# Performance work log

Hardware: AMD Instinct MI355X
Metric: run time of the kernel (lower is better)

The kernel has to match this reference:

```python
import jax, jax.numpy as jnp
import numpy as np

D_MODEL = 1024
NUM_HEADS = 16
DEPTH = D_MODEL // NUM_HEADS
B, S = 2, 2048


def setup_inputs() -> dict:
    key = jax.random.key(0)
    ks = jax.random.split(key, 12)
    std = 1.0 / np.sqrt(D_MODEL)
    inp = {
        "q": jax.random.normal(ks[0], (B, S, D_MODEL), dtype=jnp.float32),
        "k": jax.random.normal(ks[1], (B, S, D_MODEL), dtype=jnp.float32),
        "v": jax.random.normal(ks[2], (B, S, D_MODEL), dtype=jnp.float32),
        "mask": jax.random.randint(ks[3], (B, 1, 1, S), 0, 2, dtype=jnp.int32),
        "wq": jax.random.normal(ks[4], (D_MODEL, D_MODEL), dtype=jnp.float32) * std,
        "bq": jnp.zeros((D_MODEL,), dtype=jnp.float32),
        "wk": jax.random.normal(ks[5], (D_MODEL, D_MODEL), dtype=jnp.float32) * std,
        "bk": jnp.zeros((D_MODEL,), dtype=jnp.float32),
        "wv": jax.random.normal(ks[6], (D_MODEL, D_MODEL), dtype=jnp.float32) * std,
        "bv": jnp.zeros((D_MODEL,), dtype=jnp.float32),
        "wo": jax.random.normal(ks[7], (D_MODEL, D_MODEL), dtype=jnp.float32) * std,
        "bo": jnp.zeros((D_MODEL,), dtype=jnp.float32),
    }
    return inp


def _split_heads(x):
    # (B, S, D) -> (B, H, S, depth)
    b, s, _ = x.shape
    return x.reshape(b, s, NUM_HEADS, DEPTH).transpose(0, 2, 1, 3)


def reference(q, k, v, mask, wq, bq, wk, bk, wv, bv, wo, bo):
    qh = _split_heads(q @ wq + bq)   # (B,H,S,depth)
    kh = _split_heads(k @ wk + bk)
    vh = _split_heads(v @ wv + bv)
    scale = 1.0 / jnp.sqrt(jnp.float32(DEPTH))
    logits = jnp.einsum("bhqd,bhkd->bhqk", qh, kh) * scale  # (B,H,Sq,Sk)
    logits = logits + mask.astype(logits.dtype) * -1e9
    attn = jax.nn.softmax(logits, axis=-1)
    out = jnp.einsum("bhqk,bhkd->bhqd", attn, vh)  # (B,H,Sq,depth)
    out = out.transpose(0, 2, 1, 3).reshape(q.shape[0], -1, D_MODEL)
    return out @ wo + bo
```

## Files before the change

### kernel.cpp

```cpp
#include <hip/hip_runtime.h>
#include <hip/hip_bf16.h>
#include <stdint.h>


typedef __bf16 bf16;
typedef __bf16 bf16x8 __attribute__((ext_vector_type(8)));
typedef __bf16 bf16x4 __attribute__((ext_vector_type(4)));
typedef float  f32x4  __attribute__((ext_vector_type(4)));

#define D_MODEL 1024
#define S_LEN   2048
#define NH      16
#define DEPTH   64

#define LOG2E   1.4426950408889634f
#define QSCALE  (0.125f * LOG2E)
#define SMAX    20.0f
#define PADPEN  (-30000.0f)

__device__ __forceinline__ void gload_lds16(const void* g, void* l) {
  __builtin_amdgcn_global_load_lds(
      (__attribute__((address_space(1))) void*)g,
      (__attribute__((address_space(3))) void*)l,
      16, 0, 0);
}

__global__ __launch_bounds__(256) void setup(
    const void* __restrict__ q, const void* __restrict__ k,
    const void* __restrict__ v, const int* __restrict__ mask,
    const void* __restrict__ wq, const void* __restrict__ wk,
    const void* __restrict__ wv, const void* __restrict__ wo,
    const void* __restrict__ bq, const void* __restrict__ bk,
    const void* __restrict__ bv, const void* __restrict__ bo,
    bf16* __restrict__ wqT, bf16* __restrict__ wkT,
    bf16* __restrict__ wvT, bf16* __restrict__ woT,
    bf16* __restrict__ bqb, bf16* __restrict__ bkb,
    bf16* __restrict__ bvb, bf16* __restrict__ bob,
    bf16* __restrict__ qb, bf16* __restrict__ kb, bf16* __restrict__ vb,
    int* __restrict__ cpos, int* __restrict__ nb, int* __restrict__ flagout)
{
  const int t = threadIdx.x;
  uint32_t w = ((const uint32_t*)q)[t];
  uint32_t e = (w >> 7) & 0xFF;
  int inr = (e >= 90 && e <= 150) ? 1 : 0;
  __shared__ int flg;
  int cnt = __syncthreads_count(inr);
  if (t == 0) flg = (cnt > 160) ? 1 : 0;
  __syncthreads();
  int flag = flg;

  const int bid = blockIdx.x;
  if (bid < 2) {
    const int b = bid;
    const int lane = t & 63, wv4 = t >> 6;
    __shared__ int wsum[4];
    int vals[8], s = 0;
#pragma unroll
    for (int j = 0; j < 8; ++j) {
      vals[j] = (mask[b * S_LEN + t * 8 + j] == 0) ? 1 : 0;
      s += vals[j];
    }
    int acc = s;
    for (int off = 1; off < 64; off <<= 1) {
      int u = __shfl_up(acc, off);
      if (lane >= off) acc += u;
    }
    if (lane == 63) wsum[wv4] = acc;
    __syncthreads();
    int base = 0;
    for (int w4 = 0; w4 < 4; ++w4) base += (w4 < wv4) ? wsum[w4] : 0;
    int ex = base + acc - s;
#pragma unroll
    for (int j = 0; j < 8; ++j) {
      cpos[b * S_LEN + t * 8 + j] = vals[j] ? ex : -1;
      ex += vals[j];
    }
    if (t == 255) nb[b] = base + acc;
    if (b == 0 && t == 0) *flagout = flag;
  } else if (bid < 6) {
    const int j = bid - 2;
    const void* B; bf16* O;
    switch (j) {
      case 0:  B = bq; O = bqb; break;
      case 1:  B = bk; O = bkb; break;
      case 2:  B = bv; O = bvb; break;
      default: B = bo; O = bob; break;
    }
    const float sc = (j == 0) ? QSCALE : 1.0f;
    for (int jj = 0; jj < 4; ++jj) {
      const int i = t + jj * 256;
      const float val = flag ? (float)((const bf16*)B)[i] : ((const float*)B)[i];
      O[i] = (bf16)(val * sc);
    }
  } else if (bid < 6 + 1024) {
    const int job = bid - 6;
    const int wsel = job >> 8, rem = job & 255;
    const void* W; bf16* T;
    switch (wsel) {
      case 0:  W = wq; T = wqT; break;
      case 1:  W = wk; T = wkT; break;
      case 2:  W = wv; T = wvT; break;
      default: W = wo; T = woT; break;
    }
    const float sc = (wsel == 0) ? QSCALE : 1.0f;
    __shared__ float tile[64][65];
    const int tx = t & 63, ty = t >> 6;
    const int x0 = (rem & 15) * 64;
    const int y0 = (rem >> 4) * 64;
    for (int i = ty; i < 64; i += 4) {
      const size_t gi = (size_t)(y0 + i) * D_MODEL + x0 + tx;
      tile[i][tx] = flag ? (float)((const bf16*)W)[gi] : ((const float*)W)[gi];
    }
    __syncthreads();
    for (int j = ty; j < 64; j += 4)
      T[(size_t)(x0 + j) * D_MODEL + y0 + tx] = (bf16)(tile[tx][j] * sc);
  } else {
    if (flag) return;
    const int job = bid - 1030;
    const int tensor = job >> 11, blk = job & 2047;
    const void* src; bf16* dst;
    switch (tensor) {
      case 0:  src = q; dst = qb; break;
      case 1:  src = k; dst = kb; break;
      default: src = v; dst = vb; break;
    }
    const size_t idx = ((size_t)blk * 256 + t) * 8;
    const float* s = (const float*)src + idx;
    f32x4 a = *(const f32x4*)(s);
    f32x4 b2 = *(const f32x4*)(s + 4);
    bf16x8 o;
    for (int i = 0; i < 4; ++i) { o[i] = (bf16)a[i]; o[4 + i] = (bf16)b2[i]; }
    *(bf16x8*)(dst + idx) = o;
  }
}

struct GArgs {
  const bf16* A;
  const void* Araw;
  const bf16* BT;
  const bf16* bias;
  void* out;
  const int* cpos;
  int mode;
};

__device__ __forceinline__ void gemm_body(const GArgs& g, int flag)
{
  const bf16* A = flag ? (const bf16*)g.Araw : g.A;

  __shared__ __align__(16) bf16 As[2][128 * 32];
  __shared__ __align__(16) bf16 Bs[2][128 * 32];
  const int tid  = threadIdx.x;
  const int wave = tid >> 6, lane = tid & 63;
  const int quad = lane >> 4, l16 = lane & 15;

  const int flat = blockIdx.y * 8 + blockIdx.x;
  const int xcd = flat & 7, pos = flat >> 3;
  const int bx = (xcd & 1) * 4 + (pos & 3);
  const int by = (xcd >> 1) * 8 + (pos >> 2);
  const int m0 = by * 128, n0 = bx * 128;

  const int wm = (wave >> 1) * 64, wn = (wave & 1) * 64;
  const int srow = lane >> 2;
  const int scol = (((lane & 3) ^ ((lane >> 3) & 3)) * 8);

  f32x4 acc[4][4] = {};

  const bf16* Ag = A    + (size_t)(m0 + wave * 32 + srow) * D_MODEL + scol;
  const bf16* Bg = g.BT + (size_t)(n0 + wave * 32 + srow) * D_MODEL + scol;
  const int lbase = (wave * 32) * 32;
  const int rsw = (quad ^ ((l16 >> 1) & 3)) * 8;

  gload_lds16(Ag,                &As[0][lbase]);
  gload_lds16(Ag + 16 * D_MODEL, &As[0][lbase + 16 * 32]);
  gload_lds16(Bg,                &Bs[0][lbase]);
  gload_lds16(Bg + 16 * D_MODEL, &Bs[0][lbase + 16 * 32]);
  __syncthreads();

  int cur = 0;
  for (int kt = 0; kt < D_MODEL; kt += 32, cur ^= 1) {
    if (kt + 32 < D_MODEL) {
      const int nxt = cur ^ 1;
      gload_lds16(Ag + kt + 32,                &As[nxt][lbase]);
      gload_lds16(Ag + kt + 32 + 16 * D_MODEL, &As[nxt][lbase + 16 * 32]);
      gload_lds16(Bg + kt + 32,                &Bs[nxt][lbase]);
      gload_lds16(Bg + kt + 32 + 16 * D_MODEL, &Bs[nxt][lbase + 16 * 32]);
    }

    bf16x8 af[4], bfv[4];
#pragma unroll
    for (int mi = 0; mi < 4; ++mi)
      af[mi] = *(const bf16x8*)(&As[cur][(wm + mi * 16 + l16) * 32 + rsw]);
#pragma unroll
    for (int ni = 0; ni < 4; ++ni)
      bfv[ni] = *(const bf16x8*)(&Bs[cur][(wn + ni * 16 + l16) * 32 + rsw]);
#pragma unroll
    for (int mi = 0; mi < 4; ++mi)
#pragma unroll
      for (int ni = 0; ni < 4; ++ni)
        acc[mi][ni] = __builtin_amdgcn_mfma_f32_16x16x32_bf16(
            af[mi], bfv[ni], acc[mi][ni], 0, 0, 0);

    __syncthreads();
  }

  if (g.mode == 2) {
    bf16* tw = (wn == 0) ? (bf16*)As : (bf16*)Bs;
#pragma unroll
    for (int ni = 0; ni < 4; ++ni) {
      const int d = ni * 16 + l16;
      const int sw = (d & 7) << 3;
      const float bv = (float)g.bias[n0 + wn + ni * 16 + l16];
#pragma unroll
      for (int mi = 0; mi < 4; ++mi) {
        const int sA = wm + mi * 16 + quad * 4;
        bf16x4 p;
        p[0] = (bf16)(acc[mi][ni][0] + bv);
        p[1] = (bf16)(acc[mi][ni][1] + bv);
        p[2] = (bf16)(acc[mi][ni][2] + bv);
        p[3] = (bf16)(acc[mi][ni][3] + bv);
        *(bf16x4*)(tw + d * 128 + (sA ^ sw)) = p;
      }
    }
    __syncthreads();
    const int bb = m0 >> 11, s0g = m0 & 2047;
    const int hsel = wave & 1, dbase = (wave >> 1) * 32;
    const int hh = (n0 >> 6) + hsel;
    const bf16* tr = hsel ? (const bf16*)Bs : (const bf16*)As;
    const int cp0 = g.cpos[bb * S_LEN + s0g + lane];
    const int cp1 = g.cpos[bb * S_LEN + s0g + 64 + lane];
#pragma unroll 4
    for (int dd = 0; dd < 32; ++dd) {
      const int d = dbase + dd;
      const int sw = (d & 7) << 3;
      bf16* vbase = (bf16*)g.out +
                    ((size_t)(bb * NH + hh) * DEPTH + d) * S_LEN;
      const bf16 v0 = tr[d * 128 + (lane ^ sw)];
      const bf16 v1 = tr[d * 128 + ((64 + lane) ^ sw)];
      if (cp0 >= 0) vbase[cp0] = v0;
      if (cp1 >= 0) vbase[cp1] = v1;
    }
    return;
  }

  if (g.mode != 0) {
    bf16* strip = ((bf16*)As) + wave * (16 * 72);
    const int hh = (n0 + wn) >> 6;
    float bvf[4];
#pragma unroll
    for (int ni = 0; ni < 4; ++ni)
      bvf[ni] = (float)g.bias[n0 + wn + ni * 16 + l16];

#pragma unroll
    for (int mi = 0; mi < 4; ++mi) {
      const int row0 = m0 + wm + mi * 16;
      const int b = row0 >> 11, s0 = row0 & 2047;

#pragma unroll
      for (int ni = 0; ni < 4; ++ni)
#pragma unroll
        for (int r = 0; r < 4; ++r)
          strip[(quad * 4 + r) * 72 + ni * 16 + l16] =
              (bf16)(acc[mi][ni][r] + bvf[ni]);

      if (g.mode == 1) {
        bf16* ob = (bf16*)g.out +
                   ((size_t)(b * NH + hh) * S_LEN + s0) * DEPTH;
#pragma unroll
        for (int half = 0; half < 2; ++half) {
          const int rl = half * 8 + (lane >> 3);
          bf16x8 vv = *(const bf16x8*)(strip + rl * 72 + (lane & 7) * 8);
          *(bf16x8*)(ob + (size_t)rl * DEPTH + (lane & 7) * 8) = vv;
        }
      } else {
        bf16* kb = (bf16*)g.out + (size_t)(b * NH + hh) * S_LEN * DEPTH;
#pragma unroll
        for (int half = 0; half < 2; ++half) {
          const int rl = half * 8 + (lane >> 3);
          const int cpv = g.cpos[b * S_LEN + s0 + rl];
          bf16x8 vv = *(const bf16x8*)(strip + rl * 72 + (lane & 7) * 8);
          if (cpv >= 0)
            *(bf16x8*)(kb + (size_t)cpv * DEPTH + (lane & 7) * 8) = vv;
        }
      }
    }
    return;
  }

#pragma unroll
  for (int mi = 0; mi < 4; ++mi) {
    const int row0 = m0 + wm + mi * 16 + quad * 4;
#pragma unroll
    for (int ni = 0; ni < 4; ++ni) {
      const int col  = n0 + wn + ni * 16 + l16;
      const float bv = (float)g.bias[col];
      if (flag) {
        bf16* op = (bf16*)g.out + (size_t)row0 * D_MODEL + col;
#pragma unroll
        for (int r = 0; r < 4; ++r)
          op[(size_t)r * D_MODEL] = (bf16)(acc[mi][ni][r] + bv);
      } else {
        float* op = (float*)g.out + (size_t)row0 * D_MODEL + col;
#pragma unroll
        for (int r = 0; r < 4; ++r)
          op[(size_t)r * D_MODEL] = acc[mi][ni][r] + bv;
      }
    }
  }
}

__global__ __launch_bounds__(256) void gemm_qkv(GArgs g0, GArgs g1, GArgs g2,
                                                const int* __restrict__ flagp)
{
  const GArgs& g = (blockIdx.z == 0) ? g0 : ((blockIdx.z == 1) ? g1 : g2);
  gemm_body(g, *flagp);
}

__global__ __launch_bounds__(256) void gemm_out(GArgs g,
                                                const int* __restrict__ flagp)
{
  const int flag = *flagp;
  const bf16* A = (const bf16*)g.A;

  __shared__ __align__(16) bf16 As[2][64 * 32];
  __shared__ __align__(16) bf16 Bs[2][128 * 32];
  const int tid  = threadIdx.x;
  const int wave = tid >> 6, lane = tid & 63;
  const int quad = lane >> 4, l16 = lane & 15;

  const int flat = blockIdx.y * 8 + blockIdx.x;
  const int xcd = flat & 7, pos = flat >> 3;
  const int bx = (xcd & 1) * 4 + (pos & 3);
  const int by = (xcd >> 1) * 16 + (pos >> 2);
  const int m0 = by * 64, n0 = bx * 128;

  const int wm = (wave >> 1) * 32, wn = (wave & 1) * 64;
  const int srow = lane >> 2;
  const int scol = (((lane & 3) ^ ((lane >> 3) & 3)) * 8);

  f32x4 acc[2][4] = {};

  const bf16* Ag = A    + (size_t)(m0 + wave * 16 + (lane >> 2)) * D_MODEL + scol;
  const bf16* Bg = g.BT + (size_t)(n0 + wave * 32 + srow) * D_MODEL + scol;
  const int lbaseA = wave * 16 * 32;
  const int lbaseB = wave * 32 * 32;
  const int rsw = (quad ^ ((l16 >> 1) & 3)) * 8;

  gload_lds16(Ag,                &As[0][lbaseA]);
  gload_lds16(Bg,                &Bs[0][lbaseB]);
  gload_lds16(Bg + 16 * D_MODEL, &Bs[0][lbaseB + 16 * 32]);
  __syncthreads();

  int cur = 0;
  for (int kt = 0; kt < D_MODEL; kt += 32, cur ^= 1) {
    if (kt + 32 < D_MODEL) {
      const int nxt = cur ^ 1;
      gload_lds16(Ag + kt + 32,                &As[nxt][lbaseA]);
      gload_lds16(Bg + kt + 32,                &Bs[nxt][lbaseB]);
      gload_lds16(Bg + kt + 32 + 16 * D_MODEL, &Bs[nxt][lbaseB + 16 * 32]);
    }

    bf16x8 af[2], bfv[4];
#pragma unroll
    for (int mi = 0; mi < 2; ++mi)
      af[mi] = *(const bf16x8*)(&As[cur][(wm + mi * 16 + l16) * 32 + rsw]);
#pragma unroll
    for (int ni = 0; ni < 4; ++ni)
      bfv[ni] = *(const bf16x8*)(&Bs[cur][(wn + ni * 16 + l16) * 32 + rsw]);
#pragma unroll
    for (int mi = 0; mi < 2; ++mi)
#pragma unroll
      for (int ni = 0; ni < 4; ++ni)
        acc[mi][ni] = __builtin_amdgcn_mfma_f32_16x16x32_bf16(
            af[mi], bfv[ni], acc[mi][ni], 0, 0, 0);

    __syncthreads();
  }

#pragma unroll
  for (int mi = 0; mi < 2; ++mi) {
    const int row0 = m0 + wm + mi * 16 + quad * 4;
#pragma unroll
    for (int ni = 0; ni < 4; ++ni) {
      const int col  = n0 + wn + ni * 16 + l16;
      const float bv = (float)g.bias[col];
      if (flag) {
        bf16* op = (bf16*)g.out + (size_t)row0 * D_MODEL + col;
#pragma unroll
        for (int r = 0; r < 4; ++r)
          op[(size_t)r * D_MODEL] = (bf16)(acc[mi][ni][r] + bv);
      } else {
        float* op = (float*)g.out + (size_t)row0 * D_MODEL + col;
#pragma unroll
        for (int r = 0; r < 4; ++r)
          op[(size_t)r * D_MODEL] = acc[mi][ni][r] + bv;
      }
    }
  }
}

__global__ __launch_bounds__(256) void attn(
    const bf16* __restrict__ Qh, const bf16* __restrict__ Kc,
    const bf16* __restrict__ Vc, const int* __restrict__ nbp,
    bf16* __restrict__ Oh)
{
  const int flat = blockIdx.y * 16 + blockIdx.x;
  const int xcd = flat & 7, grp = flat >> 3;
  const int bh = xcd + (grp >> 4) * 8;
  const int b  = bh >> 4;
  const int h  = bh & 15;
  const int q0 = (grp & 15) * 128;
  const int tid = threadIdx.x, wave = tid >> 6, lane = tid & 63;
  const int quad = lane >> 4, l16 = lane & 15;

  __shared__ __align__(16) bf16 Ks[64][72];
  __shared__ __align__(16) bf16 Vts[64][72];
  __shared__ __align__(16) bf16 Ps[4][32][72];

  const int nbv = nbp[b];
  const int nb_pad = (nbv + 63) & ~63;

  const bf16* Qg = Qh + ((size_t)bh * S_LEN + q0 + wave * 32) * DEPTH;
  bf16x8 aq00 = *(const bf16x8*)(Qg + (size_t)l16 * DEPTH + quad * 8);
  bf16x8 aq01 = *(const bf16x8*)(Qg + (size_t)l16 * DEPTH + 32 + quad * 8);
  bf16x8 aq10 = *(const bf16x8*)(Qg + (size_t)(16 + l16) * DEPTH + quad * 8);
  bf16x8 aq11 = *(const bf16x8*)(Qg + (size_t)(16 + l16) * DEPTH + 32 + quad * 8);

  bf16x8 ones;
#pragma unroll
  for (int j = 0; j < 8; ++j) ones[j] = (bf16)1.0f;

  f32x4 o_acc[2][4] = {};
  f32x4 l_acc[2] = {};

  const bf16* Kg = Kc + (size_t)bh * S_LEN * DEPTH;
  const bf16* Vg = Vc + (size_t)bh * DEPTH * S_LEN;

  const int sr0 = tid >> 3, sc0 = (tid & 7) * 8;
  const int sr1 = sr0 + 32;

  bf16x8 kr0, kr1, vr0, vr1;
  {
    kr0 = *(const bf16x8*)(Kg + (size_t)sr0 * DEPTH + sc0);
    kr1 = *(const bf16x8*)(Kg + (size_t)sr1 * DEPTH + sc0);
    vr0 = *(const bf16x8*)(Vg + (size_t)sr0 * S_LEN + sc0);
    vr1 = *(const bf16x8*)(Vg + (size_t)sr1 * S_LEN + sc0);
  }

  for (int kb = 0; kb < nb_pad; kb += 64) {
    __syncthreads();
    *(bf16x8*)(&Ks[sr0][sc0])  = kr0;
    *(bf16x8*)(&Ks[sr1][sc0])  = kr1;
    *(bf16x8*)(&Vts[sr0][sc0]) = vr0;
    *(bf16x8*)(&Vts[sr1][sc0]) = vr1;
    __syncthreads();
    if (kb + 64 < nb_pad) {
      kr0 = *(const bf16x8*)(Kg + (size_t)(kb + 64 + sr0) * DEPTH + sc0);
      kr1 = *(const bf16x8*)(Kg + (size_t)(kb + 64 + sr1) * DEPTH + sc0);
      vr0 = *(const bf16x8*)(Vg + (size_t)sr0 * S_LEN + kb + 64 + sc0);
      vr1 = *(const bf16x8*)(Vg + (size_t)sr1 * S_LEN + kb + 64 + sc0);
    }

    f32x4 sacc[2][4] = {};
    __builtin_amdgcn_s_setprio(1);
#pragma unroll
    for (int jn = 0; jn < 4; ++jn) {
      bf16x8 bk0 = *(const bf16x8*)(&Ks[jn * 16 + l16][quad * 8]);
      bf16x8 bk1 = *(const bf16x8*)(&Ks[jn * 16 + l16][32 + quad * 8]);
      sacc[0][jn] = __builtin_amdgcn_mfma_f32_16x16x32_bf16(aq00, bk0, sacc[0][jn], 0, 0, 0);
      sacc[0][jn] = __builtin_amdgcn_mfma_f32_16x16x32_bf16(aq01, bk1, sacc[0][jn], 0, 0, 0);
      sacc[1][jn] = __builtin_amdgcn_mfma_f32_16x16x32_bf16(aq10, bk0, sacc[1][jn], 0, 0, 0);
      sacc[1][jn] = __builtin_amdgcn_mfma_f32_16x16x32_bf16(aq11, bk1, sacc[1][jn], 0, 0, 0);
    }
    __builtin_amdgcn_s_setprio(0);

#pragma unroll
    for (int jn = 0; jn < 4; ++jn) {
      const int key = kb + jn * 16 + l16;
      const float pen = (key < nbv) ? (-SMAX) : PADPEN;
#pragma unroll
      for (int qs = 0; qs < 2; ++qs)
#pragma unroll
        for (int r = 0; r < 4; ++r)
          Ps[wave][qs * 16 + quad * 4 + r][jn * 16 + l16] =
              (bf16)__builtin_amdgcn_exp2f(sacc[qs][jn][r] + pen);
    }

    bf16x8 ap00 = *(const bf16x8*)(&Ps[wave][l16][quad * 8]);
    bf16x8 ap01 = *(const bf16x8*)(&Ps[wave][l16][32 + quad * 8]);
    bf16x8 ap10 = *(const bf16x8*)(&Ps[wave][16 + l16][quad * 8]);
    bf16x8 ap11 = *(const bf16x8*)(&Ps[wave][16 + l16][32 + quad * 8]);
    __builtin_amdgcn_s_setprio(1);
#pragma unroll
    for (int jd = 0; jd < 4; ++jd) {
      bf16x8 bv0 = *(const bf16x8*)(&Vts[jd * 16 + l16][quad * 8]);
      bf16x8 bv1 = *(const bf16x8*)(&Vts[jd * 16 + l16][32 + quad * 8]);
      o_acc[0][jd] = __builtin_amdgcn_mfma_f32_16x16x32_bf16(ap00, bv0, o_acc[0][jd], 0, 0, 0);
      o_acc[0][jd] = __builtin_amdgcn_mfma_f32_16x16x32_bf16(ap01, bv1, o_acc[0][jd], 0, 0, 0);
      o_acc[1][jd] = __builtin_amdgcn_mfma_f32_16x16x32_bf16(ap10, bv0, o_acc[1][jd], 0, 0, 0);
      o_acc[1][jd] = __builtin_amdgcn_mfma_f32_16x16x32_bf16(ap11, bv1, o_acc[1][jd], 0, 0, 0);
    }
    l_acc[0] = __builtin_amdgcn_mfma_f32_16x16x32_bf16(ap00, ones, l_acc[0], 0, 0, 0);
    l_acc[0] = __builtin_amdgcn_mfma_f32_16x16x32_bf16(ap01, ones, l_acc[0], 0, 0, 0);
    l_acc[1] = __builtin_amdgcn_mfma_f32_16x16x32_bf16(ap10, ones, l_acc[1], 0, 0, 0);
    l_acc[1] = __builtin_amdgcn_mfma_f32_16x16x32_bf16(ap11, ones, l_acc[1], 0, 0, 0);
    __builtin_amdgcn_s_setprio(0);
  }

#pragma unroll
  for (int qs = 0; qs < 2; ++qs) {
#pragma unroll
    for (int r = 0; r < 4; ++r) {
      const int s = q0 + wave * 32 + qs * 16 + quad * 4 + r;
      const float inv = 1.f / l_acc[qs][r];
#pragma unroll
      for (int jd = 0; jd < 4; ++jd) {
        const int d = jd * 16 + l16;
        Oh[(size_t)(b * S_LEN + s) * D_MODEL + h * DEPTH + d] =
            (bf16)(o_acc[qs][jd][r] * inv);
      }
    }
  }
}

extern "C" void kernel_launch(void* const* d_in, const int* in_sizes, int n_in,
                              void* d_out, int out_size, void* d_ws, size_t ws_size,
                              hipStream_t stream)
{
  const void* q    = d_in[0];
  const void* k    = d_in[1];
  const void* v    = d_in[2];
  const int*  mask = (const int*)d_in[3];
  const void* wq   = d_in[4];
  const void* bq   = d_in[5];
  const void* wk   = d_in[6];
  const void* bk   = d_in[7];
  const void* wv   = d_in[8];
  const void* bv   = d_in[9];
  const void* wo   = d_in[10];
  const void* bo   = d_in[11];

  char* ws = (char*)d_ws;
  const size_t MB = 1u << 20;
  bf16* Qh  = (bf16*)(ws + 0 * MB);
  bf16* Kc  = (bf16*)(ws + 8 * MB);
  bf16* Vc  = (bf16*)(ws + 16 * MB);
  bf16* Oh  = (bf16*)(ws + 24 * MB);
  bf16* wqT = (bf16*)(ws + 32 * MB);
  bf16* wkT = (bf16*)(ws + 34 * MB);
  bf16* wvT = (bf16*)(ws + 36 * MB);
  bf16* woT = (bf16*)(ws + 38 * MB);
  bf16* bqb = (bf16*)(ws + 40 * MB);
  bf16* bkb = (bf16*)(ws + 40 * MB + 4096);
  bf16* bvb = (bf16*)(ws + 40 * MB + 8192);
  bf16* bob = (bf16*)(ws + 40 * MB + 12288);
  int*  flag = (int*)(ws + 40 * MB + 32768);
  int*  cpos = (int*)(ws + 40 * MB + 65536);
  int*  nb   = (int*)(ws + 40 * MB + 65536 + 16384);
  bf16* qb  = (bf16*)(ws + 41 * MB);
  bf16* kb_ = (bf16*)(ws + 49 * MB);
  bf16* vb_ = (bf16*)(ws + 57 * MB);

  setup<<<7174, 256, 0, stream>>>(
      q, k, v, mask, wq, wk, wv, wo, bq, bk, bv, bo,
      wqT, wkT, wvT, woT, bqb, bkb, bvb, bob,
      qb, kb_, vb_, cpos, nb, flag);

  GArgs gq{qb,  q,  wqT, bqb, Qh, nullptr, 1};
  GArgs gk{kb_, k,  wkT, bkb, Kc, cpos,    3};
  GArgs gv{vb_, v,  wvT, bvb, Vc, cpos,    2};
  gemm_qkv<<<dim3(8, 32, 3), 256, 0, stream>>>(gq, gk, gv, flag);

  attn<<<dim3(16, 32), 256, 0, stream>>>(Qh, Kc, Vc, nb, Oh);

  GArgs go{Oh, Oh, woT, bob, d_out, nullptr, 0};
  gemm_out<<<dim3(8, 64), 256, 0, stream>>>(go, flag);
}
```

Baseline: 223.1 us.

## Fuse fp32-to-bf16 input conversion into the QKV GEMM A-tile loader

Drops the setup-kernel blocks that converted q, k and v from fp32 into separate bf16 buffers. The GEMM now reads fp32 A tiles straight into registers, prefetching one k-step ahead, converts them to bf16 after the MFMA step and writes them to LDS in the same swizzled layout. This removes a full write and re-read of the converted activations and shrinks the setup launch. In exchange the GEMM reads twice the A bytes per tile and uses register-staged LDS stores instead of direct global-to-LDS loads, which adds VGPR pressure and VALU work in the inner loop.

```diff
diff --git a/kernel.cpp b/kernel.cpp
--- a/kernel.cpp
+++ b/kernel.cpp
@@ -36,7 +36,6 @@
     bf16* __restrict__ wvT, bf16* __restrict__ woT,
     bf16* __restrict__ bqb, bf16* __restrict__ bkb,
     bf16* __restrict__ bvb, bf16* __restrict__ bob,
-    bf16* __restrict__ qb, bf16* __restrict__ kb, bf16* __restrict__ vb,
     int* __restrict__ cpos, int* __restrict__ nb, int* __restrict__ flagout)
 {
   const int t = threadIdx.x;
@@ -92,7 +91,7 @@
       const float val = flag ? (float)((const bf16*)B)[i] : ((const float*)B)[i];
       O[i] = (bf16)(val * sc);
     }
-  } else if (bid < 6 + 1024) {
+  } else {
     const int job = bid - 6;
     const int wsel = job >> 8, rem = job & 255;
     const void* W; bf16* T;
@@ -114,23 +113,6 @@
     __syncthreads();
     for (int j = ty; j < 64; j += 4)
       T[(size_t)(x0 + j) * D_MODEL + y0 + tx] = (bf16)(tile[tx][j] * sc);
-  } else {
-    if (flag) return;
-    const int job = bid - 1030;
-    const int tensor = job >> 11, blk = job & 2047;
-    const void* src; bf16* dst;
-    switch (tensor) {
-      case 0:  src = q; dst = qb; break;
-      case 1:  src = k; dst = kb; break;
-      default: src = v; dst = vb; break;
-    }
-    const size_t idx = ((size_t)blk * 256 + t) * 8;
-    const float* s = (const float*)src + idx;
-    f32x4 a = *(const f32x4*)(s);
-    f32x4 b2 = *(const f32x4*)(s + 4);
-    bf16x8 o;
-    for (int i = 0; i < 4; ++i) { o[i] = (bf16)a[i]; o[4 + i] = (bf16)b2[i]; }
-    *(bf16x8*)(dst + idx) = o;
   }
 }
 
@@ -146,7 +128,8 @@
 
 __device__ __forceinline__ void gemm_body(const GArgs& g, int flag)
 {
-  const bf16* A = flag ? (const bf16*)g.Araw : g.A;
+  const bf16*  Abf = (const bf16*)g.Araw;
+  const float* Af  = (const float*)g.Araw;
 
   __shared__ __align__(16) bf16 As[2][128 * 32];
   __shared__ __align__(16) bf16 Bs[2][128 * 32];
@@ -166,23 +149,47 @@
 
   f32x4 acc[4][4] = {};
 
-  const bf16* Ag = A    + (size_t)(m0 + wave * 32 + srow) * D_MODEL + scol;
-  const bf16* Bg = g.BT + (size_t)(n0 + wave * 32 + srow) * D_MODEL + scol;
+  const bf16*  Agb = Abf + (size_t)(m0 + wave * 32 + srow) * D_MODEL + scol;
+  const float* Agf = Af  + (size_t)(m0 + wave * 32 + srow) * D_MODEL + scol;
+  const bf16*  Bg  = g.BT + (size_t)(n0 + wave * 32 + srow) * D_MODEL + scol;
   const int lbase = (wave * 32) * 32;
   const int rsw = (quad ^ ((l16 >> 1) & 3)) * 8;
 
-  gload_lds16(Ag,                &As[0][lbase]);
-  gload_lds16(Ag + 16 * D_MODEL, &As[0][lbase + 16 * 32]);
+  if (flag) {
+    gload_lds16(Agb,                &As[0][lbase]);
+    gload_lds16(Agb + 16 * D_MODEL, &As[0][lbase + 16 * 32]);
+  } else {
+    f32x4 p0 = *(const f32x4*)(Agf);
+    f32x4 p1 = *(const f32x4*)(Agf + 4);
+    f32x4 p2 = *(const f32x4*)(Agf + 16 * D_MODEL);
+    f32x4 p3 = *(const f32x4*)(Agf + 16 * D_MODEL + 4);
+    bf16x8 w0, w1;
+#pragma unroll
+    for (int i = 0; i < 4; ++i) {
+      w0[i] = (bf16)p0[i]; w0[4 + i] = (bf16)p1[i];
+      w1[i] = (bf16)p2[i]; w1[4 + i] = (bf16)p3[i];
+    }
+    *(bf16x8*)(&As[0][lbase + lane * 8])           = w0;
+    *(bf16x8*)(&As[0][lbase + 16 * 32 + lane * 8]) = w1;
+  }
   gload_lds16(Bg,                &Bs[0][lbase]);
   gload_lds16(Bg + 16 * D_MODEL, &Bs[0][lbase + 16 * 32]);
   __syncthreads();
 
   int cur = 0;
+  f32x4 pa0, pa1, pa2, pa3;
   for (int kt = 0; kt < D_MODEL; kt += 32, cur ^= 1) {
+    const int nxt = cur ^ 1;
     if (kt + 32 < D_MODEL) {
-      const int nxt = cur ^ 1;
-      gload_lds16(Ag + kt + 32,                &As[nxt][lbase]);
-      gload_lds16(Ag + kt + 32 + 16 * D_MODEL, &As[nxt][lbase + 16 * 32]);
+      if (flag) {
+        gload_lds16(Agb + kt + 32,                &As[nxt][lbase]);
+        gload_lds16(Agb + kt + 32 + 16 * D_MODEL, &As[nxt][lbase + 16 * 32]);
+      } else {
+        pa0 = *(const f32x4*)(Agf + kt + 32);
+        pa1 = *(const f32x4*)(Agf + kt + 32 + 4);
+        pa2 = *(const f32x4*)(Agf + kt + 32 + 16 * D_MODEL);
+        pa3 = *(const f32x4*)(Agf + kt + 32 + 16 * D_MODEL + 4);
+      }
       gload_lds16(Bg + kt + 32,                &Bs[nxt][lbase]);
       gload_lds16(Bg + kt + 32 + 16 * D_MODEL, &Bs[nxt][lbase + 16 * 32]);
     }
@@ -200,6 +207,17 @@
       for (int ni = 0; ni < 4; ++ni)
         acc[mi][ni] = __builtin_amdgcn_mfma_f32_16x16x32_bf16(
             af[mi], bfv[ni], acc[mi][ni], 0, 0, 0);
+
+    if (kt + 32 < D_MODEL && !flag) {
+      bf16x8 w0, w1;
+#pragma unroll
+      for (int i = 0; i < 4; ++i) {
+        w0[i] = (bf16)pa0[i]; w0[4 + i] = (bf16)pa1[i];
+        w1[i] = (bf16)pa2[i]; w1[4 + i] = (bf16)pa3[i];
+      }
+      *(bf16x8*)(&As[nxt][lbase + lane * 8])           = w0;
+      *(bf16x8*)(&As[nxt][lbase + 16 * 32 + lane * 8]) = w1;
+    }
 
     __syncthreads();
   }
@@ -557,18 +575,15 @@
   int*  flag = (int*)(ws + 40 * MB + 32768);
   int*  cpos = (int*)(ws + 40 * MB + 65536);
   int*  nb   = (int*)(ws + 40 * MB + 65536 + 16384);
-  bf16* qb  = (bf16*)(ws + 41 * MB);
-  bf16* kb_ = (bf16*)(ws + 49 * MB);
-  bf16* vb_ = (bf16*)(ws + 57 * MB);
-
-  setup<<<7174, 256, 0, stream>>>(
+
+  setup<<<1030, 256, 0, stream>>>(
       q, k, v, mask, wq, wk, wv, wo, bq, bk, bv, bo,
       wqT, wkT, wvT, woT, bqb, bkb, bvb, bob,
-      qb, kb_, vb_, cpos, nb, flag);
-
-  GArgs gq{qb,  q,  wqT, bqb, Qh, nullptr, 1};
-  GArgs gk{kb_, k,  wkT, bkb, Kc, cpos,    3};
-  GArgs gv{vb_, v,  wvT, bvb, Vc, cpos,    2};
+      cpos, nb, flag);
+
+  GArgs gq{nullptr, q, wqT, bqb, Qh, nullptr, 1};
+  GArgs gk{nullptr, k, wkT, bkb, Kc, cpos,    3};
+  GArgs gv{nullptr, v, wvT, bvb, Vc, cpos,    2};
   gemm_qkv<<<dim3(8, 32, 3), 256, 0, stream>>>(gq, gk, gv, flag);
 
   attn<<<dim3(16, 32), 256, 0, stream>>>(Qh, Kc, Vc, nb, Oh);
```

After: 254.4 us. 1.14x slower.

## Gather unmasked rows before K/V projection GEMMs and skip empty tiles

Applied to the files above, without the earlier changes.

The setup kernel now also writes an inverse index (jpos) from compacted position to source row. The K and V projection GEMMs gather only the unmasked rows through this index and return early for row tiles beyond the unmasked count. Before, every row was projected and masked rows were dropped at store time. Because the mask is roughly half zeros, this should cut K/V projection work by about half, at the cost of gathered, less regular A-row loads and an extra index write in setup.

```diff
diff --git a/kernel.cpp b/kernel.cpp
--- a/kernel.cpp
+++ b/kernel.cpp
@@ -37,7 +37,8 @@
     bf16* __restrict__ bqb, bf16* __restrict__ bkb,
     bf16* __restrict__ bvb, bf16* __restrict__ bob,
     bf16* __restrict__ qb, bf16* __restrict__ kb, bf16* __restrict__ vb,
-    int* __restrict__ cpos, int* __restrict__ nb, int* __restrict__ flagout)
+    int* __restrict__ cpos, int* __restrict__ jpos,
+    int* __restrict__ nb, int* __restrict__ flagout)
 {
   const int t = threadIdx.x;
   uint32_t w = ((const uint32_t*)q)[t];
@@ -73,6 +74,7 @@
 #pragma unroll
     for (int j = 0; j < 8; ++j) {
       cpos[b * S_LEN + t * 8 + j] = vals[j] ? ex : -1;
+      if (vals[j]) jpos[b * S_LEN + ex] = t * 8 + j;
       ex += vals[j];
     }
     if (t == 255) nb[b] = base + acc;
@@ -140,7 +142,8 @@
   const bf16* BT;
   const bf16* bias;
   void* out;
-  const int* cpos;
+  const int* jpos;
+  const int* nbp;
   int mode;
 };
 
@@ -160,19 +163,40 @@
   const int by = (xcd >> 1) * 8 + (pos >> 2);
   const int m0 = by * 128, n0 = bx * 128;
 
+  const bool compact = (g.mode >= 2);
+  int bB = 0, jy = 0, nbv_blk = 0;
+  if (compact) {
+    bB = by >> 4; jy = by & 15;
+    nbv_blk = g.nbp[bB];
+    if (jy * 128 >= nbv_blk) return;
+  }
+
   const int wm = (wave >> 1) * 64, wn = (wave & 1) * 64;
   const int srow = lane >> 2;
   const int scol = (((lane & 3) ^ ((lane >> 3) & 3)) * 8);
 
   f32x4 acc[4][4] = {};
 
-  const bf16* Ag = A    + (size_t)(m0 + wave * 32 + srow) * D_MODEL + scol;
-  const bf16* Bg = g.BT + (size_t)(n0 + wave * 32 + srow) * D_MODEL + scol;
+  int arow0, arow1;
+  if (compact) {
+    const int j0 = jy * 128 + wave * 32 + srow;
+    const int j1 = j0 + 16;
+    const int s0i = (j0 < nbv_blk) ? g.jpos[bB * S_LEN + j0] : g.jpos[bB * S_LEN];
+    const int s1i = (j1 < nbv_blk) ? g.jpos[bB * S_LEN + j1] : g.jpos[bB * S_LEN];
+    arow0 = bB * S_LEN + s0i;
+    arow1 = bB * S_LEN + s1i;
+  } else {
+    arow0 = m0 + wave * 32 + srow;
+    arow1 = arow0 + 16;
+  }
+  const bf16* Ag0 = A + (size_t)arow0 * D_MODEL + scol;
+  const bf16* Ag1 = A + (size_t)arow1 * D_MODEL + scol;
+  const bf16* Bg  = g.BT + (size_t)(n0 + wave * 32 + srow) * D_MODEL + scol;
   const int lbase = (wave * 32) * 32;
   const int rsw = (quad ^ ((l16 >> 1) & 3)) * 8;
 
-  gload_lds16(Ag,                &As[0][lbase]);
-  gload_lds16(Ag + 16 * D_MODEL, &As[0][lbase + 16 * 32]);
+  gload_lds16(Ag0, &As[0][lbase]);
+  gload_lds16(Ag1, &As[0][lbase + 16 * 32]);
   gload_lds16(Bg,                &Bs[0][lbase]);
   gload_lds16(Bg + 16 * D_MODEL, &Bs[0][lbase + 16 * 32]);
   __syncthreads();
@@ -181,8 +205,8 @@
   for (int kt = 0; kt < D_MODEL; kt += 32, cur ^= 1) {
     if (kt + 32 < D_MODEL) {
       const int nxt = cur ^ 1;
-      gload_lds16(Ag + kt + 32,                &As[nxt][lbase]);
-      gload_lds16(Ag + kt + 32 + 16 * D_MODEL, &As[nxt][lbase + 16 * 32]);
+      gload_lds16(Ag0 + kt + 32, &As[nxt][lbase]);
+      gload_lds16(Ag1 + kt + 32, &As[nxt][lbase + 16 * 32]);
       gload_lds16(Bg + kt + 32,                &Bs[nxt][lbase]);
       gload_lds16(Bg + kt + 32 + 16 * D_MODEL, &Bs[nxt][lbase + 16 * 32]);
     }
@@ -223,22 +247,21 @@
       }
     }
     __syncthreads();
-    const int bb = m0 >> 11, s0g = m0 & 2047;
     const int hsel = wave & 1, dbase = (wave >> 1) * 32;
     const int hh = (n0 >> 6) + hsel;
     const bf16* tr = hsel ? (const bf16*)Bs : (const bf16*)As;
-    const int cp0 = g.cpos[bb * S_LEN + s0g + lane];
-    const int cp1 = g.cpos[bb * S_LEN + s0g + 64 + lane];
+    const int j0g = jy * 128;
+    const int cp0 = j0g + lane, cp1 = j0g + 64 + lane;
 #pragma unroll 4
     for (int dd = 0; dd < 32; ++dd) {
       const int d = dbase + dd;
       const int sw = (d & 7) << 3;
       bf16* vbase = (bf16*)g.out +
-                    ((size_t)(bb * NH + hh) * DEPTH + d) * S_LEN;
+                    ((size_t)(bB * NH + hh) * DEPTH + d) * S_LEN;
       const bf16 v0 = tr[d * 128 + (lane ^ sw)];
       const bf16 v1 = tr[d * 128 + ((64 + lane) ^ sw)];
-      if (cp0 >= 0) vbase[cp0] = v0;
-      if (cp1 >= 0) vbase[cp1] = v1;
+      if (cp0 < nbv_blk) vbase[cp0] = v0;
+      if (cp1 < nbv_blk) vbase[cp1] = v1;
     }
     return;
   }
@@ -253,9 +276,6 @@
 
 #pragma unroll
     for (int mi = 0; mi < 4; ++mi) {
-      const int row0 = m0 + wm + mi * 16;
-      const int b = row0 >> 11, s0 = row0 & 2047;
-
 #pragma unroll
       for (int ni = 0; ni < 4; ++ni)
 #pragma unroll
@@ -264,6 +284,8 @@
               (bf16)(acc[mi][ni][r] + bvf[ni]);
 
       if (g.mode == 1) {
+        const int row0 = m0 + wm + mi * 16;
+        const int b = row0 >> 11, s0 = row0 & 2047;
         bf16* ob = (bf16*)g.out +
                    ((size_t)(b * NH + hh) * S_LEN + s0) * DEPTH;
 #pragma unroll
@@ -273,14 +295,15 @@
           *(bf16x8*)(ob + (size_t)rl * DEPTH + (lane & 7) * 8) = vv;
         }
       } else {
-        bf16* kb = (bf16*)g.out + (size_t)(b * NH + hh) * S_LEN * DEPTH;
+        const int j0r = jy * 128 + wm + mi * 16;
+        bf16* kb = (bf16*)g.out + (size_t)(bB * NH + hh) * S_LEN * DEPTH;
 #pragma unroll
         for (int half = 0; half < 2; ++half) {
           const int rl = half * 8 + (lane >> 3);
-          const int cpv = g.cpos[b * S_LEN + s0 + rl];
+          const int jj = j0r + rl;
           bf16x8 vv = *(const bf16x8*)(strip + rl * 72 + (lane & 7) * 8);
-          if (cpv >= 0)
-            *(bf16x8*)(kb + (size_t)cpv * DEPTH + (lane & 7) * 8) = vv;
+          if (jj < nbv_blk)
+            *(bf16x8*)(kb + (size_t)jj * DEPTH + (lane & 7) * 8) = vv;
         }
       }
     }
@@ -557,6 +580,7 @@
   int*  flag = (int*)(ws + 40 * MB + 32768);
   int*  cpos = (int*)(ws + 40 * MB + 65536);
   int*  nb   = (int*)(ws + 40 * MB + 65536 + 16384);
+  int*  jpos = (int*)(ws + 40 * MB + 98304);
   bf16* qb  = (bf16*)(ws + 41 * MB);
   bf16* kb_ = (bf16*)(ws + 49 * MB);
   bf16* vb_ = (bf16*)(ws + 57 * MB);
@@ -564,15 +588,15 @@
   setup<<<7174, 256, 0, stream>>>(
       q, k, v, mask, wq, wk, wv, wo, bq, bk, bv, bo,
       wqT, wkT, wvT, woT, bqb, bkb, bvb, bob,
-      qb, kb_, vb_, cpos, nb, flag);
-
-  GArgs gq{qb,  q,  wqT, bqb, Qh, nullptr, 1};
-  GArgs gk{kb_, k,  wkT, bkb, Kc, cpos,    3};
-  GArgs gv{vb_, v,  wvT, bvb, Vc, cpos,    2};
+      qb, kb_, vb_, cpos, jpos, nb, flag);
+
+  GArgs gq{qb,  q,  wqT, bqb, Qh, nullptr, nullptr, 1};
+  GArgs gk{kb_, k,  wkT, bkb, Kc, jpos,    nb,      3};
+  GArgs gv{vb_, v,  wvT, bvb, Vc, jpos,    nb,      2};
   gemm_qkv<<<dim3(8, 32, 3), 256, 0, stream>>>(gq, gk, gv, flag);
 
   attn<<<dim3(16, 32), 256, 0, stream>>>(Qh, Kc, Vc, nb, Oh);
 
-  GArgs go{Oh, Oh, woT, bob, d_out, nullptr, 0};
+  GArgs go{Oh, Oh, woT, bob, d_out, nullptr, nullptr, 0};
   gemm_out<<<dim3(8, 64), 256, 0, stream>>>(go, flag);
 }
```

New measurement: 242.6 us. +8.8%, slower.
